# Optimization experiments

Measured on AMD Instinct MI355X. Metric: run time of the kernel, lower is better.

Reference implementation:

```python
import jax, jax.numpy as jnp
import numpy as np

N_NODES = 50000
N_EDGES = 400000
IN_FEATS = 1433
HID = 384
EMB = 256
N_CLS = 7


def setup_inputs() -> dict:
    key = jax.random.key(0)
    ks = jax.random.split(key, 9)
    features = jax.random.normal(ks[0], (N_NODES, IN_FEATS), jnp.float32)
    edge_src = jax.random.randint(ks[1], (N_EDGES,), 0, N_NODES)
    edge_dst = jax.random.randint(ks[2], (N_EDGES,), 0, N_NODES)
    W1 = jax.random.normal(ks[3], (IN_FEATS, HID), jnp.float32) * 0.02
    b1 = jnp.zeros((HID,), jnp.float32)
    W2 = jax.random.normal(ks[4], (HID, EMB), jnp.float32) * 0.02
    b2 = jnp.zeros((EMB,), jnp.float32)
    Wc = jax.random.normal(ks[5], (EMB, N_CLS), jnp.float32) * 0.02
    bc = jnp.zeros((N_CLS,), jnp.float32)
    return {"features": features, "edge_src": edge_src, "edge_dst": edge_dst,
            "W1": W1, "b1": b1, "W2": W2, "b2": b2, "Wc": Wc, "bc": bc}


def reference(features, edge_src, edge_dst, W1, b1, W2, b2, Wc, bc):
    N = features.shape[0]
    ones = jnp.ones(edge_src.shape[0], features.dtype)
    deg_out = jax.ops.segment_sum(ones, edge_src, num_segments=N)
    deg_in = jax.ops.segment_sum(ones, edge_dst, num_segments=N)
    inv_s = jax.lax.rsqrt(jnp.maximum(deg_out, 1.0))  # D_src^{-1/2}
    inv_d = jax.lax.rsqrt(jnp.maximum(deg_in, 1.0))   # D_dst^{-1/2}

    def gconv(x, W, b):
        # DGL GraphConv, norm='both', weight applied first (in_feats > out_feats)
        h = (x @ W) * inv_s[:, None]
        agg = jax.ops.segment_sum(h[edge_src], edge_dst, num_segments=N)
        return agg * inv_d[:, None] + b

    h = jax.nn.relu(gconv(features, W1, b1))
    h = gconv(h, W2, b2)
    return h @ Wc + bc  # [N, 7] logits
```

## Files before the change

kernel.cpp:

```cpp
#include <hip/hip_runtime.h>
#include <math.h>
#include <stdint.h>

constexpr int NNODES = 50000;
constexpr int NEDGES = 400000;
constexpr int INF = 1433;
constexpr int KP1 = 1440;
constexpr int MP1 = 50048;
constexpr int NRB = MP1 / 128;
constexpr int NKT1 = KP1 / 32;
constexpr int HID = 384;
constexpr int NKT2 = HID / 32;
constexpr int EMB = 256;
constexpr int NCLS = 7;
constexpr int NSB = (NNODES + 255) / 256;

typedef __attribute__((ext_vector_type(8))) short bf16x8_t;
typedef __attribute__((ext_vector_type(4))) float f32x4_t;

typedef __attribute__((address_space(3))) uint32_t lds_u32_t;
typedef const __attribute__((address_space(1))) uint32_t glb_u32_t;

__global__ void degree_kernel(const int* __restrict__ src, const int* __restrict__ dst,
                              int* __restrict__ dout, int* __restrict__ din, int E) {
  int i = blockIdx.x * blockDim.x + threadIdx.x;
  int stride = gridDim.x * blockDim.x;
  for (; i < E; i += stride) {
    atomicAdd(&dout[src[i]], 1);
    atomicAdd(&din[dst[i]], 1);
  }
}

__global__ void inv_kernel(const int* __restrict__ dout, const int* __restrict__ din,
                           float* __restrict__ inv_s, float* __restrict__ inv_d, int N) {
  int i = blockIdx.x * blockDim.x + threadIdx.x;
  if (i < N) {
    inv_s[i] = 1.0f / sqrtf(fmaxf((float)dout[i], 1.0f));
    inv_d[i] = 1.0f / sqrtf(fmaxf((float)din[i], 1.0f));
  }
}

__global__ __launch_bounds__(256)
void scan_block(const int* __restrict__ deg, int* __restrict__ off,
                int* __restrict__ bsum, int N) {
  __shared__ int buf[256];
  int i = blockIdx.x * 256 + threadIdx.x;
  int v = (i < N) ? deg[i] : 0;
  buf[threadIdx.x] = v;
  __syncthreads();
  #pragma unroll
  for (int d = 1; d < 256; d <<= 1) {
    int t = (threadIdx.x >= d) ? buf[threadIdx.x - d] : 0;
    __syncthreads();
    buf[threadIdx.x] += t;
    __syncthreads();
  }
  if (i < N) off[i] = buf[threadIdx.x] - v;
  if (threadIdx.x == 255) bsum[blockIdx.x] = buf[255];
}

__global__ __launch_bounds__(256)
void scan_tops(const int* __restrict__ bsum, int* __restrict__ boff,
               int* __restrict__ off, int nb, int N) {
  __shared__ int buf[256];
  int v = (threadIdx.x < nb) ? bsum[threadIdx.x] : 0;
  buf[threadIdx.x] = v;
  __syncthreads();
  #pragma unroll
  for (int d = 1; d < 256; d <<= 1) {
    int t = (threadIdx.x >= d) ? buf[threadIdx.x - d] : 0;
    __syncthreads();
    buf[threadIdx.x] += t;
    __syncthreads();
  }
  if (threadIdx.x < nb) boff[threadIdx.x] = buf[threadIdx.x] - v;
  if (threadIdx.x == 255) off[N] = buf[255];
}

__global__ __launch_bounds__(256)
void scan_add(const int* __restrict__ boff, int* __restrict__ off, int N) {
  int i = blockIdx.x * 256 + threadIdx.x;
  if (i < N) off[i] += boff[blockIdx.x];
}

__global__ void fill_csr(const int* __restrict__ src, const int* __restrict__ dst,
                         const int* __restrict__ off, int* __restrict__ cursor,
                         int* __restrict__ csr_src, int E) {
  int i = blockIdx.x * blockDim.x + threadIdx.x;
  int stride = gridDim.x * blockDim.x;
  for (; i < E; i += stride) {
    int d = dst[i];
    int p = atomicAdd(&cursor[d], 1);
    csr_src[off[d] + p] = src[i];
  }
}

__device__ __forceinline__ uint32_t split_pack(float v) {
  uint32_t u = __float_as_uint(v);
  float hiF = __uint_as_float(u & 0xFFFF0000u);
  uint32_t u2 = __float_as_uint(v - hiF);
  return (u2 & 0xFFFF0000u) | (u >> 16);
}

__global__ void convA(const float* __restrict__ A, uint32_t* __restrict__ Ap) {
  int k4 = blockIdx.x * 256 + threadIdx.x;
  int r = blockIdx.y;
  if (k4 >= KP1 / 4) return;
  int k = k4 * 4;
  uint4 o = {0, 0, 0, 0};
  if (r < NNODES) {
    const float* row = A + (size_t)r * INF;
    if (k + 3 < INF) {
      float a0 = row[k], a1 = row[k + 1], a2 = row[k + 2], a3 = row[k + 3];
      o.x = split_pack(a0); o.y = split_pack(a1); o.z = split_pack(a2); o.w = split_pack(a3);
    } else {
      if (k + 0 < INF) o.x = split_pack(row[k + 0]);
      if (k + 1 < INF) o.y = split_pack(row[k + 1]);
      if (k + 2 < INF) o.z = split_pack(row[k + 2]);
      if (k + 3 < INF) o.w = split_pack(row[k + 3]);
    }
  }
  *(uint4*)&Ap[(size_t)r * KP1 + k] = o;
}

template<int KDIM, int NDIM, int NKTILES>
__global__ void convB(const float* __restrict__ W, char* __restrict__ Bp) {
  int T = blockIdx.x, cb = blockIdx.y;
  int kk = threadIdx.x & 31, c0 = threadIdx.x >> 5;
  char* tile = Bp + ((size_t)cb * NKTILES + T) * 16384;
  int gk = T * 32 + kk;
  #pragma unroll
  for (int i = 0; i < 16; ++i) {
    int c = c0 + i * 8;
    float v = (gk < KDIM) ? W[(size_t)gk * NDIM + cb * 128 + c] : 0.f;
    uint32_t p = split_pack(v);
    int bo = (c * 64 + kk * 2) ^ ((c & 7) << 4);
    *(ushort*)(tile + bo)        = (ushort)(p & 0xFFFFu);
    *(ushort*)(tile + 8192 + bo) = (ushort)(p >> 16);
  }
}

template<int KPD, int NOUT, int NCOLB, int NKTILES>
__global__ __launch_bounds__(256, 2)
void gemm_mfma(const uint32_t* __restrict__ Ap, const char* __restrict__ Bp,
               float* __restrict__ C, const float* __restrict__ scale)
{
  __shared__ __align__(16) char sA[16384];
  __shared__ __align__(16) char sB[16384];

  constexpr int NWG = NCOLB * NRB;
  constexpr int q = NWG / 8, rr = NWG % 8;
  int orig = blockIdx.x;
  int xcd = orig & 7, sub = orig >> 3;
  int logical = (xcd < rr ? xcd * (q + 1) : rr * (q + 1) + (xcd - rr) * q) + sub;
  int bx = logical % NCOLB;
  int by = logical / NCOLB;
  const int row0 = by * 128, col0 = bx * 128;

  const int tid = threadIdx.x;
  const int w = tid >> 6, l = tid & 63;
  const int wr = w >> 1, wc = w & 1;
  const int lane15 = l & 15, kg = l >> 4;

  uint32_t a_off[4];
  #pragma unroll
  for (int i = 0; i < 4; ++i) {
    int p = w * 4096 + i * 1024 + l * 16;
    int r = p >> 7;
    int kb = (p & 127) ^ ((r & 7) << 4);
    a_off[i] = (uint32_t)(row0 + r) * (KPD * 4) + kb;
  }
  const char* Ab = (const char*)Ap;
  const char* Btile = Bp + (size_t)(bx * NKTILES) * 16384;

  f32x4_t acc[4][4];
  #pragma unroll
  for (int mi = 0; mi < 4; ++mi)
    #pragma unroll
    for (int ni = 0; ni < 4; ++ni) acc[mi][ni] = {0.f, 0.f, 0.f, 0.f};

  for (int T = 0; T < NKTILES; ++T) {
    #pragma unroll
    for (int i = 0; i < 4; ++i) {
      __builtin_amdgcn_global_load_lds(
          (glb_u32_t*)(Ab + (size_t)(a_off[i] + (uint32_t)T * 128u)),
          (lds_u32_t*)(sA + w * 4096 + i * 1024), 16, 0, 0);
    }
    #pragma unroll
    for (int i = 0; i < 4; ++i) {
      int p = w * 4096 + i * 1024;
      __builtin_amdgcn_global_load_lds(
          (glb_u32_t*)(Btile + (size_t)T * 16384 + p + l * 16),
          (lds_u32_t*)(sB + p), 16, 0, 0);
    }
    __syncthreads();

    bf16x8_t bh[4], bl[4];
    #pragma unroll
    for (int ni = 0; ni < 4; ++ni) {
      int c = wc * 64 + ni * 16 + lane15;
      int bo = (c * 64 + kg * 16) ^ ((c & 7) << 4);
      bh[ni] = *(const bf16x8_t*)(sB + bo);
      bl[ni] = *(const bf16x8_t*)(sB + 8192 + bo);
    }
    #pragma unroll
    for (int mi = 0; mi < 4; ++mi) {
      int ra = wr * 64 + mi * 16 + lane15;
      int a0 = (ra * 128 + kg * 32) ^ ((ra & 7) << 4);
      uint4 d0 = *(const uint4*)(sA + a0);
      uint4 d1 = *(const uint4*)(sA + (a0 ^ 16));
      union { uint32_t u[4]; bf16x8_t v; } th, tl;
      th.u[0] = (d0.x & 0xFFFFu) | (d0.y << 16);
      th.u[1] = (d0.z & 0xFFFFu) | (d0.w << 16);
      th.u[2] = (d1.x & 0xFFFFu) | (d1.y << 16);
      th.u[3] = (d1.z & 0xFFFFu) | (d1.w << 16);
      tl.u[0] = (d0.x >> 16) | (d0.y & 0xFFFF0000u);
      tl.u[1] = (d0.z >> 16) | (d0.w & 0xFFFF0000u);
      tl.u[2] = (d1.x >> 16) | (d1.y & 0xFFFF0000u);
      tl.u[3] = (d1.z >> 16) | (d1.w & 0xFFFF0000u);
      #pragma unroll
      for (int ni = 0; ni < 4; ++ni) {
        acc[mi][ni] = __builtin_amdgcn_mfma_f32_16x16x32_bf16(th.v, bh[ni], acc[mi][ni], 0, 0, 0);
        acc[mi][ni] = __builtin_amdgcn_mfma_f32_16x16x32_bf16(th.v, bl[ni], acc[mi][ni], 0, 0, 0);
        acc[mi][ni] = __builtin_amdgcn_mfma_f32_16x16x32_bf16(tl.v, bh[ni], acc[mi][ni], 0, 0, 0);
      }
    }
    __syncthreads();
  }

  #pragma unroll
  for (int mi = 0; mi < 4; ++mi) {
    #pragma unroll
    for (int j = 0; j < 4; ++j) {
      int gr = row0 + wr * 64 + mi * 16 + kg * 4 + j;
      if (gr >= NNODES) continue;
      float s = scale[gr];
      #pragma unroll
      for (int ni = 0; ni < 4; ++ni) {
        int gc = col0 + wc * 64 + ni * 16 + lane15;
        C[(size_t)gr * NOUT + gc] = acc[mi][ni][j] * s;
      }
    }
  }
}

template<int BK>
__global__ __launch_bounds__(256)
void gemm_scale(const float* __restrict__ A, const float* __restrict__ B,
                float* __restrict__ C, const float* __restrict__ scale,
                int M, int N, int K)
{
  constexpr int BM = 128, BN = 128;
  constexpr int LDA = BM + 4;
  constexpr int LDB = BN + 4;
  __shared__ float As[BK][LDA];
  __shared__ float Bs[BK][LDB];

  const int tid = threadIdx.x;
  const int tx = tid & 15;
  const int ty = tid >> 4;
  const int row0 = blockIdx.y * BM;
  const int col0 = blockIdx.x * BN;

  float acc[8][8];
  #pragma unroll
  for (int i = 0; i < 8; ++i)
    #pragma unroll
    for (int j = 0; j < 8; ++j) acc[i][j] = 0.f;

  for (int kt = 0; kt < K; kt += BK) {
    #pragma unroll
    for (int p = 0; p < BM / 16; ++p) {
      int r = (tid >> 4) + p * 16;
      int k = tid & 15;
      int gr = row0 + r, gk = kt + k;
      float v = 0.f;
      if (gr < M && gk < K) v = A[(size_t)gr * K + gk];
      As[k][r] = v;
    }
    #pragma unroll
    for (int p = 0; p < BK / 8; ++p) {
      int r = (tid >> 5) + p * 8;
      int c4 = (tid & 31) * 4;
      int gk = kt + r;
      float4 v = {0.f, 0.f, 0.f, 0.f};
      if (gk < K) v = *(const float4*)&B[(size_t)gk * N + col0 + c4];
      *(float4*)&Bs[r][c4] = v;
    }
    __syncthreads();
    #pragma unroll
    for (int k = 0; k < BK; ++k) {
      float4 a0 = *(const float4*)&As[k][ty * 8];
      float4 a1 = *(const float4*)&As[k][ty * 8 + 4];
      float4 b0 = *(const float4*)&Bs[k][tx * 8];
      float4 b1 = *(const float4*)&Bs[k][tx * 8 + 4];
      float av[8] = {a0.x, a0.y, a0.z, a0.w, a1.x, a1.y, a1.z, a1.w};
      float bv[8] = {b0.x, b0.y, b0.z, b0.w, b1.x, b1.y, b1.z, b1.w};
      #pragma unroll
      for (int i = 0; i < 8; ++i)
        #pragma unroll
        for (int j = 0; j < 8; ++j)
          acc[i][j] = fmaf(av[i], bv[j], acc[i][j]);
    }
    __syncthreads();
  }
  #pragma unroll
  for (int i = 0; i < 8; ++i) {
    int gr = row0 + ty * 8 + i;
    if (gr >= M) continue;
    float s = scale[gr];
    #pragma unroll
    for (int j = 0; j < 8; j += 4) {
      float4 v = {acc[i][j] * s, acc[i][j + 1] * s, acc[i][j + 2] * s, acc[i][j + 3] * s};
      *(float4*)&C[(size_t)gr * N + col0 + tx * 8 + j] = v;
    }
  }
}

template<int NF, bool RELU>
__global__ __launch_bounds__(256)
void gather_nodes(const int* __restrict__ off, const int* __restrict__ csr_src,
                  const float* __restrict__ h, const float* __restrict__ inv_d,
                  const float* __restrict__ bias, float* __restrict__ outbuf, int N)
{
  int node = blockIdx.x * 4 + (threadIdx.x >> 6);
  int lane = threadIdx.x & 63;
  if (node >= N) return;
  constexpr int NI = NF / 128;
  float2 acc[NI];
  #pragma unroll
  for (int i = 0; i < NI; ++i) acc[i] = {0.f, 0.f};

  int e0 = off[node], e1 = off[node + 1];
  for (int e = e0; e < e1; ++e) {
    const float* hr = h + (size_t)csr_src[e] * NF;
    #pragma unroll
    for (int i = 0; i < NI; ++i) {
      float2 v = *(const float2*)&hr[lane * 2 + i * 128];
      acc[i].x += v.x; acc[i].y += v.y;
    }
  }
  float s = inv_d[node];
  float* orow = outbuf + (size_t)node * NF;
  #pragma unroll
  for (int i = 0; i < NI; ++i) {
    int f = lane * 2 + i * 128;
    float2 v;
    v.x = fmaf(acc[i].x, s, bias[f]);
    v.y = fmaf(acc[i].y, s, bias[f + 1]);
    if (RELU) { v.x = fmaxf(v.x, 0.f); v.y = fmaxf(v.y, 0.f); }
    *(float2*)&orow[f] = v;
  }
}

__global__ __launch_bounds__(256)
void gather_pack(const int* __restrict__ off, const int* __restrict__ csr_src,
                 const float* __restrict__ h, const float* __restrict__ inv_d,
                 const float* __restrict__ bias, uint32_t* __restrict__ outp, int N)
{
  int node = blockIdx.x * 4 + (threadIdx.x >> 6);
  int lane = threadIdx.x & 63;
  if (node >= N) return;
  float2 acc[3];
  #pragma unroll
  for (int i = 0; i < 3; ++i) acc[i] = {0.f, 0.f};

  int e0 = off[node], e1 = off[node + 1];
  int e = e0;
  for (; e + 4 <= e1; e += 4) {
    const float* r0 = h + (size_t)csr_src[e + 0] * HID;
    const float* r1 = h + (size_t)csr_src[e + 1] * HID;
    const float* r2 = h + (size_t)csr_src[e + 2] * HID;
    const float* r3 = h + (size_t)csr_src[e + 3] * HID;
    #pragma unroll
    for (int i = 0; i < 3; ++i) {
      int f = lane * 2 + i * 128;
      float2 v0 = *(const float2*)&r0[f];
      float2 v1 = *(const float2*)&r1[f];
      float2 v2 = *(const float2*)&r2[f];
      float2 v3 = *(const float2*)&r3[f];
      acc[i].x += (v0.x + v1.x) + (v2.x + v3.x);
      acc[i].y += (v0.y + v1.y) + (v2.y + v3.y);
    }
  }
  for (; e < e1; ++e) {
    const float* hr = h + (size_t)csr_src[e] * HID;
    #pragma unroll
    for (int i = 0; i < 3; ++i) {
      float2 v = *(const float2*)&hr[lane * 2 + i * 128];
      acc[i].x += v.x; acc[i].y += v.y;
    }
  }
  float s = inv_d[node];
  uint32_t* orow = outp + (size_t)node * HID;
  #pragma unroll
  for (int i = 0; i < 3; ++i) {
    int f = lane * 2 + i * 128;
    float vx = fmaxf(fmaf(acc[i].x, s, bias[f]), 0.f);
    float vy = fmaxf(fmaf(acc[i].y, s, bias[f + 1]), 0.f);
    uint2 o = {split_pack(vx), split_pack(vy)};
    *(uint2*)&orow[f] = o;
  }
}

__global__ __launch_bounds__(256)
void gather_classifier(const int* __restrict__ off, const int* __restrict__ csr_src,
                       const float* __restrict__ h, const float* __restrict__ inv_d,
                       const float* __restrict__ b2, const float* __restrict__ Wc,
                       const float* __restrict__ bc, float* __restrict__ out, int N)
{
  __shared__ float sWc[EMB * NCLS];
  for (int i = threadIdx.x; i < EMB * NCLS; i += 256) sWc[i] = Wc[i];
  __syncthreads();

  int node = blockIdx.x * 4 + (threadIdx.x >> 6);
  int lane = threadIdx.x & 63;
  if (node >= N) return;

  float2 acc[2] = {{0.f, 0.f}, {0.f, 0.f}};
  int e0 = off[node], e1 = off[node + 1];
  int e = e0;
  for (; e + 4 <= e1; e += 4) {
    const float* r0 = h + (size_t)csr_src[e + 0] * EMB;
    const float* r1 = h + (size_t)csr_src[e + 1] * EMB;
    const float* r2 = h + (size_t)csr_src[e + 2] * EMB;
    const float* r3 = h + (size_t)csr_src[e + 3] * EMB;
    #pragma unroll
    for (int i = 0; i < 2; ++i) {
      int f = lane * 2 + i * 128;
      float2 v0 = *(const float2*)&r0[f];
      float2 v1 = *(const float2*)&r1[f];
      float2 v2 = *(const float2*)&r2[f];
      float2 v3 = *(const float2*)&r3[f];
      acc[i].x += (v0.x + v1.x) + (v2.x + v3.x);
      acc[i].y += (v0.y + v1.y) + (v2.y + v3.y);
    }
  }
  for (; e < e1; ++e) {
    const float* hr = h + (size_t)csr_src[e] * EMB;
    #pragma unroll
    for (int i = 0; i < 2; ++i) {
      float2 v = *(const float2*)&hr[lane * 2 + i * 128];
      acc[i].x += v.x; acc[i].y += v.y;
    }
  }
  float s = inv_d[node];
  float c[NCLS];
  #pragma unroll
  for (int k = 0; k < NCLS; ++k) c[k] = 0.f;
  #pragma unroll
  for (int i = 0; i < 2; ++i) {
    int f = lane * 2 + i * 128;
    float hx = fmaf(acc[i].x, s, b2[f]);
    float hy = fmaf(acc[i].y, s, b2[f + 1]);
    #pragma unroll
    for (int k = 0; k < NCLS; ++k)
      c[k] += hx * sWc[f * NCLS + k] + hy * sWc[(f + 1) * NCLS + k];
  }
  #pragma unroll
  for (int k = 0; k < NCLS; ++k) {
    float v = c[k];
    #pragma unroll
    for (int o = 32; o > 0; o >>= 1) v += __shfl_down(v, o);
    if (lane == 0) out[(size_t)node * NCLS + k] = v + bc[k];
  }
}

extern "C" void kernel_launch(void* const* d_in, const int* in_sizes, int n_in,
                              void* d_out, int out_size, void* d_ws, size_t ws_size,
                              hipStream_t stream) {
  const float* features = (const float*)d_in[0];
  const int*   esrc     = (const int*)d_in[1];
  const int*   edst     = (const int*)d_in[2];
  const float* W1       = (const float*)d_in[3];
  const float* b1       = (const float*)d_in[4];
  const float* W2       = (const float*)d_in[5];
  const float* b2       = (const float*)d_in[6];
  const float* Wc       = (const float*)d_in[7];
  const float* bc       = (const float*)d_in[8];
  float* out = (float*)d_out;

  int* deg_out = (int*)d_ws;
  int* deg_in  = deg_out + NNODES;
  int* cursor  = deg_in + NNODES;
  int* row_off = cursor + NNODES;
  int* csr_src = row_off + NNODES + 1;
  int* bsum    = csr_src + NEDGES;
  int* boff    = bsum + NSB;
  float* inv_s = (float*)(boff + NSB);
  float* inv_d = inv_s + NNODES;
  uintptr_t p16 = ((uintptr_t)(inv_d + NNODES) + 15) & ~(uintptr_t)15;
  uint32_t* hp = (uint32_t*)p16;
  float* bufA = (float*)(hp + (size_t)MP1 * HID);
  char*  Bp1  = (char*)(bufA + (size_t)NNODES * HID);
  char*  Bp2  = Bp1 + (size_t)3 * NKT1 * 16384;
  uint32_t* Ap = (uint32_t*)(Bp2 + (size_t)2 * NKT2 * 16384);

  size_t required = (uintptr_t)(Ap + (size_t)MP1 * KP1) - (uintptr_t)d_ws;
  bool use_mfma = ws_size >= required;

  hipMemsetAsync(deg_out, 0, 3 * NNODES * sizeof(int), stream);
  degree_kernel<<<1024, 256, 0, stream>>>(esrc, edst, deg_out, deg_in, NEDGES);
  inv_kernel<<<(NNODES + 255) / 256, 256, 0, stream>>>(deg_out, deg_in, inv_s, inv_d, NNODES);
  scan_block<<<NSB, 256, 0, stream>>>(deg_in, row_off, bsum, NNODES);
  scan_tops<<<1, 256, 0, stream>>>(bsum, boff, row_off, NSB, NNODES);
  scan_add<<<NSB, 256, 0, stream>>>(boff, row_off, NNODES);
  fill_csr<<<1024, 256, 0, stream>>>(esrc, edst, row_off, cursor, csr_src, NEDGES);

  if (use_mfma) {
    convA<<<dim3((KP1 / 4 + 255) / 256, MP1), 256, 0, stream>>>(features, Ap);
    convB<INF, HID, NKT1><<<dim3(NKT1, 3), 256, 0, stream>>>(W1, Bp1);
    gemm_mfma<KP1, HID, 3, NKT1><<<3 * NRB, 256, 0, stream>>>(Ap, Bp1, bufA, inv_s);
    gather_pack<<<(NNODES + 3) / 4, 256, 0, stream>>>(
        row_off, csr_src, bufA, inv_d, b1, hp, NNODES);

    convB<HID, EMB, NKT2><<<dim3(NKT2, 2), 256, 0, stream>>>(W2, Bp2);
    gemm_mfma<HID, EMB, 2, NKT2><<<2 * NRB, 256, 0, stream>>>(hp, Bp2, bufA, inv_s);
  } else {
    gemm_scale<16><<<dim3(HID / 128, (NNODES + 127) / 128), 256, 0, stream>>>(
        features, W1, bufA, inv_s, NNODES, HID, INF);
    gather_nodes<HID, true><<<(NNODES + 3) / 4, 256, 0, stream>>>(
        row_off, csr_src, bufA, inv_d, b1, (float*)hp, NNODES);
    gemm_scale<16><<<dim3(EMB / 128, (NNODES + 127) / 128), 256, 0, stream>>>(
        (float*)hp, W2, bufA, inv_s, NNODES, EMB, HID);
  }

  gather_classifier<<<(NNODES + 3) / 4, 256, 0, stream>>>(
      row_off, csr_src, bufA, inv_d, b2, Wc, bc, out, NNODES);
}
```

Baseline: 940.4 us.

## Fuse fp32-to-split-bf16 conversion of features into the first MFMA GEMM

Drops the separate convA pass, which read the whole fp32 feature matrix and wrote a padded hi/lo bf16 copy. The first GEMM now streams raw fp32 rows straight into LDS with 4-byte global_load_lds and does the hi/lo split in registers before the MFMAs. The last row block is clamped to overlap earlier rows, so the padded buffer is no longer needed. This removes a large read-and-write of the activations and a kernel launch, at the cost of four times as many narrow LDS-load instructions and extra ALU work in the GEMM inner loop. It also reads slightly past each row's end on the last K tile, which relies on the zero-padded B rows and on the final row's overrun staying in bounds.

New measurement: 839.8 us. -10.7%, faster.

```diff
diff --git a/kernel.cpp b/kernel.cpp
--- a/kernel.cpp
+++ b/kernel.cpp
@@ -102,27 +102,6 @@
   return (u2 & 0xFFFF0000u) | (u >> 16);
 }
 
-__global__ void convA(const float* __restrict__ A, uint32_t* __restrict__ Ap) {
-  int k4 = blockIdx.x * 256 + threadIdx.x;
-  int r = blockIdx.y;
-  if (k4 >= KP1 / 4) return;
-  int k = k4 * 4;
-  uint4 o = {0, 0, 0, 0};
-  if (r < NNODES) {
-    const float* row = A + (size_t)r * INF;
-    if (k + 3 < INF) {
-      float a0 = row[k], a1 = row[k + 1], a2 = row[k + 2], a3 = row[k + 3];
-      o.x = split_pack(a0); o.y = split_pack(a1); o.z = split_pack(a2); o.w = split_pack(a3);
-    } else {
-      if (k + 0 < INF) o.x = split_pack(row[k + 0]);
-      if (k + 1 < INF) o.y = split_pack(row[k + 1]);
-      if (k + 2 < INF) o.z = split_pack(row[k + 2]);
-      if (k + 3 < INF) o.w = split_pack(row[k + 3]);
-    }
-  }
-  *(uint4*)&Ap[(size_t)r * KP1 + k] = o;
-}
-
 template<int KDIM, int NDIM, int NKTILES>
 __global__ void convB(const float* __restrict__ W, char* __restrict__ Bp) {
   int T = blockIdx.x, cb = blockIdx.y;
@@ -140,9 +119,9 @@
   }
 }
 
-template<int KPD, int NOUT, int NCOLB, int NKTILES>
+template<int AROWB, int NOUT, int NCOLB, int NKTILES, bool RAW>
 __global__ __launch_bounds__(256, 2)
-void gemm_mfma(const uint32_t* __restrict__ Ap, const char* __restrict__ Bp,
+void gemm_mfma(const char* __restrict__ Ab, const char* __restrict__ Bp,
                float* __restrict__ C, const float* __restrict__ scale)
 {
   __shared__ __align__(16) char sA[16384];
@@ -155,22 +134,33 @@
   int logical = (xcd < rr ? xcd * (q + 1) : rr * (q + 1) + (xcd - rr) * q) + sub;
   int bx = logical % NCOLB;
   int by = logical / NCOLB;
-  const int row0 = by * 128, col0 = bx * 128;
+  int row0 = by * 128;
+  if (RAW) row0 = min(row0, NNODES - 128);
+  const int col0 = bx * 128;
 
   const int tid = threadIdx.x;
   const int w = tid >> 6, l = tid & 63;
   const int wr = w >> 1, wc = w & 1;
   const int lane15 = l & 15, kg = l >> 4;
 
-  uint32_t a_off[4];
-  #pragma unroll
-  for (int i = 0; i < 4; ++i) {
-    int p = w * 4096 + i * 1024 + l * 16;
-    int r = p >> 7;
-    int kb = (p & 127) ^ ((r & 7) << 4);
-    a_off[i] = (uint32_t)(row0 + r) * (KPD * 4) + kb;
-  }
-  const char* Ab = (const char*)Ap;
+  uint32_t a_base[4];
+  if constexpr (RAW) {
+    int lb = l >> 5, col4 = (l & 31) * 4;
+    #pragma unroll
+    for (int j0 = 0; j0 < 4; ++j0) {
+      int r = w * 32 + j0 * 2 + lb;
+      a_base[j0] = (uint32_t)(row0 + r) * (uint32_t)AROWB
+                 + (uint32_t)(col4 ^ ((r & 7) << 4));
+    }
+  } else {
+    #pragma unroll
+    for (int i = 0; i < 4; ++i) {
+      int p = w * 4096 + i * 1024 + l * 16;
+      int r = p >> 7;
+      int kb = (p & 127) ^ ((r & 7) << 4);
+      a_base[i] = (uint32_t)(row0 + r) * (uint32_t)AROWB + (uint32_t)kb;
+    }
+  }
   const char* Btile = Bp + (size_t)(bx * NKTILES) * 16384;
 
   f32x4_t acc[4][4];
@@ -180,11 +170,22 @@
     for (int ni = 0; ni < 4; ++ni) acc[mi][ni] = {0.f, 0.f, 0.f, 0.f};
 
   for (int T = 0; T < NKTILES; ++T) {
-    #pragma unroll
-    for (int i = 0; i < 4; ++i) {
-      __builtin_amdgcn_global_load_lds(
-          (glb_u32_t*)(Ab + (size_t)(a_off[i] + (uint32_t)T * 128u)),
-          (lds_u32_t*)(sA + w * 4096 + i * 1024), 16, 0, 0);
+    if constexpr (RAW) {
+      #pragma unroll
+      for (int jj = 0; jj < 16; ++jj) {
+        __builtin_amdgcn_global_load_lds(
+            (glb_u32_t*)(Ab + (size_t)(a_base[jj & 3]
+                                       + (uint32_t)((jj >> 2) * 8 * AROWB)
+                                       + (uint32_t)T * 128u)),
+            (lds_u32_t*)(sA + w * 4096 + jj * 256), 4, 0, 0);
+      }
+    } else {
+      #pragma unroll
+      for (int i = 0; i < 4; ++i) {
+        __builtin_amdgcn_global_load_lds(
+            (glb_u32_t*)(Ab + (size_t)(a_base[i] + (uint32_t)T * 128u)),
+            (lds_u32_t*)(sA + w * 4096 + i * 1024), 16, 0, 0);
+      }
     }
     #pragma unroll
     for (int i = 0; i < 4; ++i) {
@@ -210,14 +211,27 @@
       uint4 d0 = *(const uint4*)(sA + a0);
       uint4 d1 = *(const uint4*)(sA + (a0 ^ 16));
       union { uint32_t u[4]; bf16x8_t v; } th, tl;
-      th.u[0] = (d0.x & 0xFFFFu) | (d0.y << 16);
-      th.u[1] = (d0.z & 0xFFFFu) | (d0.w << 16);
-      th.u[2] = (d1.x & 0xFFFFu) | (d1.y << 16);
-      th.u[3] = (d1.z & 0xFFFFu) | (d1.w << 16);
-      tl.u[0] = (d0.x >> 16) | (d0.y & 0xFFFF0000u);
-      tl.u[1] = (d0.z >> 16) | (d0.w & 0xFFFF0000u);
-      tl.u[2] = (d1.x >> 16) | (d1.y & 0xFFFF0000u);
-      tl.u[3] = (d1.z >> 16) | (d1.w & 0xFFFF0000u);
+      if constexpr (RAW) {
+        uint32_t uu[8] = {d0.x, d0.y, d0.z, d0.w, d1.x, d1.y, d1.z, d1.w};
+        #pragma unroll
+        for (int pp = 0; pp < 4; ++pp) {
+          uint32_t ux = uu[2 * pp], uy = uu[2 * pp + 1];
+          uint32_t hx = ux & 0xFFFF0000u, hy = uy & 0xFFFF0000u;
+          uint32_t lx = __float_as_uint(__uint_as_float(ux) - __uint_as_float(hx));
+          uint32_t ly = __float_as_uint(__uint_as_float(uy) - __uint_as_float(hy));
+          th.u[pp] = (ux >> 16) | hy;
+          tl.u[pp] = (lx >> 16) | (ly & 0xFFFF0000u);
+        }
+      } else {
+        th.u[0] = (d0.x & 0xFFFFu) | (d0.y << 16);
+        th.u[1] = (d0.z & 0xFFFFu) | (d0.w << 16);
+        th.u[2] = (d1.x & 0xFFFFu) | (d1.y << 16);
+        th.u[3] = (d1.z & 0xFFFFu) | (d1.w << 16);
+        tl.u[0] = (d0.x >> 16) | (d0.y & 0xFFFF0000u);
+        tl.u[1] = (d0.z >> 16) | (d0.w & 0xFFFF0000u);
+        tl.u[2] = (d1.x >> 16) | (d1.y & 0xFFFF0000u);
+        tl.u[3] = (d1.z >> 16) | (d1.w & 0xFFFF0000u);
+      }
       #pragma unroll
       for (int ni = 0; ni < 4; ++ni) {
         acc[mi][ni] = __builtin_amdgcn_mfma_f32_16x16x32_bf16(th.v, bh[ni], acc[mi][ni], 0, 0, 0);
@@ -494,9 +508,8 @@
   float* bufA = (float*)(hp + (size_t)MP1 * HID);
   char*  Bp1  = (char*)(bufA + (size_t)NNODES * HID);
   char*  Bp2  = Bp1 + (size_t)3 * NKT1 * 16384;
-  uint32_t* Ap = (uint32_t*)(Bp2 + (size_t)2 * NKT2 * 16384);
-
-  size_t required = (uintptr_t)(Ap + (size_t)MP1 * KP1) - (uintptr_t)d_ws;
+
+  size_t required = (uintptr_t)(Bp2 + (size_t)2 * NKT2 * 16384) - (uintptr_t)d_ws;
   bool use_mfma = ws_size >= required;
 
   hipMemsetAsync(deg_out, 0, 3 * NNODES * sizeof(int), stream);
@@ -508,14 +521,15 @@
   fill_csr<<<1024, 256, 0, stream>>>(esrc, edst, row_off, cursor, csr_src, NEDGES);
 
   if (use_mfma) {
-    convA<<<dim3((KP1 / 4 + 255) / 256, MP1), 256, 0, stream>>>(features, Ap);
     convB<INF, HID, NKT1><<<dim3(NKT1, 3), 256, 0, stream>>>(W1, Bp1);
-    gemm_mfma<KP1, HID, 3, NKT1><<<3 * NRB, 256, 0, stream>>>(Ap, Bp1, bufA, inv_s);
+    gemm_mfma<INF * 4, HID, 3, NKT1, true><<<3 * NRB, 256, 0, stream>>>(
+        (const char*)features, Bp1, bufA, inv_s);
     gather_pack<<<(NNODES + 3) / 4, 256, 0, stream>>>(
         row_off, csr_src, bufA, inv_d, b1, hp, NNODES);
 
     convB<HID, EMB, NKT2><<<dim3(NKT2, 2), 256, 0, stream>>>(W2, Bp2);
-    gemm_mfma<HID, EMB, 2, NKT2><<<2 * NRB, 256, 0, stream>>>(hp, Bp2, bufA, inv_s);
+    gemm_mfma<HID * 4, EMB, 2, NKT2, false><<<2 * NRB, 256, 0, stream>>>(
+        (const char*)hp, Bp2, bufA, inv_s);
   } else {
     gemm_scale<16><<<dim3(HID / 128, (NNODES + 127) / 128), 256, 0, stream>>>(
         features, W1, bufA, inv_s, NNODES, HID, INF);
```
